# Optimization experiments

Hardware: AMD Instinct MI355X
Metric: run time of the kernel (lower is better)

## Reference

```python
import jax, jax.numpy as jnp
import numpy as np

HEADS = 8
KEY_DIM = 64
VALUE_DIM = 64


def setup_inputs() -> dict:
    key = jax.random.key(0)
    ks = jax.random.split(key, 6)
    B, I, O, T, S = 2, 512, 512, 2048, 2048
    E = KEY_DIM * HEADS  # 512
    Ev = VALUE_DIM * HEADS  # 512
    return {
        "x": jax.random.normal(ks[0], (B, I, T), dtype=jnp.float32),
        "y": jax.random.normal(ks[1], (B, O, S), dtype=jnp.float32),
        "mask": jnp.zeros((T, S), dtype=jnp.float32),
        "Wk": jax.random.normal(ks[2], (E, I), dtype=jnp.float32) * (I ** -0.5),
        "Wv": jax.random.normal(ks[3], (Ev, I), dtype=jnp.float32) * (I ** -0.5),
        "Wq": jax.random.normal(ks[4], (E, O), dtype=jnp.float32) * (O ** -0.5),
        "W": jax.random.normal(ks[5], (O, Ev), dtype=jnp.float32) * (Ev ** -0.5),
        "b": jnp.zeros((O,), dtype=jnp.float32),
    }


def reference(x, y, mask, Wk, Wv, Wq, W, b):
    B, I, T = x.shape
    S = y.shape[2]
    H, dk, dv = HEADS, KEY_DIM, VALUE_DIM
    scaling = dk ** -0.5
    # 1x1 Conv1d projections == channel GEMMs; reshape (B, H*d, L) -> (B*H, d, L)
    keys = jnp.einsum('ei,bit->bet', Wk, x).reshape(B * H, dk, T)
    values = jnp.einsum('ei,bit->bet', Wv, x).reshape(B * H, dv, T)
    queries = jnp.einsum('eo,bos->bes', Wq, y).reshape(B * H, dk, S)
    # scores: [B*H, T, S]
    dot = jnp.einsum('bkt,bks->bts', keys, queries)
    dot = dot + mask[None, :, :]
    # torch Softmax(1) on [bh, T, S] normalizes over T (keys axis);
    # note: scaling applied AFTER mask add, as in the original.
    attention = jax.nn.softmax(scaling * dot, axis=1)
    # weighted values: [B*H, dv, S] -> [B, H*dv, S]
    output = jnp.einsum('bvt,bts->bvs', values, attention).reshape(B, H * dv, S)
    # final Linear over channel dim applied to (B, S, H*dv)
    return jnp.einsum('bvs,ov->bso', output, W) + b
```

## Files before the change

kernel.cpp:

```cpp
#include <hip/hip_runtime.h>
#include <stdint.h>

typedef unsigned short u16;
typedef unsigned int u32;

#define B_    2
#define DK    64
#define T_    2048
#define S_    2048
#define CI    512
#define CO    512
#define E_    512

typedef short  short8 __attribute__((ext_vector_type(8)));
typedef __bf16 bf16x8 __attribute__((ext_vector_type(8)));
typedef float  f32x4  __attribute__((ext_vector_type(4)));

static __device__ __forceinline__ u16 f2bf(float f) {
    return __builtin_bit_cast(u16, (__bf16)f);
}

static __device__ __forceinline__ float bf2f(u16 h) {
    return __uint_as_float((u32)h << 16);
}

static __device__ __forceinline__ short8 ld8(const u16* p) {
    return *(const short8*)p;
}

static __device__ __forceinline__ f32x4 mfma_bf16(short8 a, short8 b, f32x4 c) {
    return __builtin_amdgcn_mfma_f32_16x16x32_bf16(
        __builtin_bit_cast(bf16x8, a), __builtin_bit_cast(bf16x8, b), c, 0, 0, 0);
}

__global__ __launch_bounds__(256) void k_prep(const float* __restrict__ x, const float* __restrict__ y,
                                              const float* __restrict__ wk, const float* __restrict__ wv,
                                              const float* __restrict__ wq, const float* __restrict__ wf,
                                              const float* __restrict__ mask,
                                              u16* __restrict__ xt, u16* __restrict__ yt,
                                              u16* __restrict__ wkb, u16* __restrict__ wvb,
                                              u16* __restrict__ wqb, u16* __restrict__ wfb,
                                              u16* __restrict__ mt, u32* __restrict__ mflag) {
    __shared__ float tile[32][33];
    int bid = blockIdx.x;
    if (bid < 4096) {
        int bx = bid & 63, by = (bid >> 6) & 15, bz = bid >> 10;
        int tsel = bz >> 1, b = bz & 1;
        const float* src = tsel ? y : x;
        u16* dst = tsel ? yt : xt;
        int t0 = bx * 32, i0 = by * 32;
        int tx = threadIdx.x & 31, ty = threadIdx.x >> 5;
#pragma unroll
        for (int r = 0; r < 4; r++)
            tile[ty + r * 8][tx] = src[(size_t)(b * CI + i0 + ty + r * 8) * T_ + t0 + tx];
        __syncthreads();
#pragma unroll
        for (int r = 0; r < 4; r++)
            dst[(size_t)(b * T_ + t0 + ty + r * 8) * CI + i0 + tx] = f2bf(tile[tx][ty + r * 8]);
    } else if (bid < 4608) {
        int off = ((bid - 4096) * 256 + threadIdx.x) * 8;
        int w = off >> 18, r = off & 262143;
        const float* s = (w == 0) ? wk : (w == 1) ? wv : (w == 2) ? wq : wf;
        u16* d = (w == 0) ? wkb : (w == 1) ? wvb : (w == 2) ? wqb : wfb;
        float4 a0 = *(const float4*)(s + r);
        float4 a1 = *(const float4*)(s + r + 4);
        short8 o;
        o[0] = f2bf(a0.x); o[1] = f2bf(a0.y); o[2] = f2bf(a0.z); o[3] = f2bf(a0.w);
        o[4] = f2bf(a1.x); o[5] = f2bf(a1.y); o[6] = f2bf(a1.z); o[7] = f2bf(a1.w);
        *(short8*)(d + r) = o;
    } else {
        int mb = bid - 4608;
        int t0 = (mb & 63) * 32, s0 = (mb >> 6) * 32;
        int tx = threadIdx.x & 31, ty = threadIdx.x >> 5;
        const float msc = 0.125f * 1.44269504088896f;
        bool nz = false;
#pragma unroll
        for (int r = 0; r < 4; r++) {
            float v = mask[(size_t)(t0 + ty + r * 8) * S_ + s0 + tx];
            tile[ty + r * 8][tx] = v;
            nz |= (v != 0.0f);
        }
        if (mflag && __any(nz) && (threadIdx.x & 63) == 0)
            atomicOr(mflag, 1u);
        __syncthreads();
#pragma unroll
        for (int r = 0; r < 4; r++)
            mt[(size_t)(s0 + ty + r * 8) * T_ + t0 + tx] = f2bf(tile[tx][ty + r * 8] * msc);
    }
}

__global__ __launch_bounds__(256) void k_proj3(const u16* __restrict__ xt, const u16* __restrict__ yt,
                                               const u16* __restrict__ wkb, const u16* __restrict__ wvb,
                                               const u16* __restrict__ wqb,
                                               u16* __restrict__ ktd, u16* __restrict__ vtd,
                                               u16* __restrict__ qtd, int p_base) {
    int bi = blockIdx.x;
    int p = p_base + (bi >> 8);
    int r = bi & 255;
    int et = r & 3, tt = r >> 2;
    int wv = threadIdx.x >> 6, lane = threadIdx.x & 63;
    int col = lane & 15, q = lane >> 4;
    int b = tt >> 5;
    int t0 = (tt & 31) * 64 + (wv >> 1) * 32;
    int e0 = et * 128 + (wv & 1) * 64;
    const u16* src = (p == 0) ? yt : xt;
    const u16* wb  = (p == 0) ? wqb : (p == 1) ? wkb : wvb;
    const u16* ap0 = src + (size_t)(b * T_ + t0 + col) * CI + q * 8;
    const u16* bp0 = wb + (size_t)(e0 + col) * CI + q * 8;
    f32x4 acc[2][4] = {};
    short8 a0 = ld8(ap0), a1 = ld8(ap0 + 16 * CI);
    short8 b0 = ld8(bp0), b1 = ld8(bp0 + 16 * CI);
    short8 b2 = ld8(bp0 + 32 * CI), b3 = ld8(bp0 + 48 * CI);
#pragma unroll
    for (int ks = 0; ks < 16; ks++) {
        short8 na0, na1, nb0, nb1, nb2, nb3;
        if (ks < 15) {
            na0 = ld8(ap0 + (ks + 1) * 32);
            na1 = ld8(ap0 + 16 * CI + (ks + 1) * 32);
            nb0 = ld8(bp0 + (ks + 1) * 32);
            nb1 = ld8(bp0 + 16 * CI + (ks + 1) * 32);
            nb2 = ld8(bp0 + 32 * CI + (ks + 1) * 32);
            nb3 = ld8(bp0 + 48 * CI + (ks + 1) * 32);
        }
        acc[0][0] = mfma_bf16(a0, b0, acc[0][0]); acc[1][0] = mfma_bf16(a1, b0, acc[1][0]);
        acc[0][1] = mfma_bf16(a0, b1, acc[0][1]); acc[1][1] = mfma_bf16(a1, b1, acc[1][1]);
        acc[0][2] = mfma_bf16(a0, b2, acc[0][2]); acc[1][2] = mfma_bf16(a1, b2, acc[1][2]);
        acc[0][3] = mfma_bf16(a0, b3, acc[0][3]); acc[1][3] = mfma_bf16(a1, b3, acc[1][3]);
        if (ks < 15) {
            a0 = na0; a1 = na1; b0 = nb0; b1 = nb1; b2 = nb2; b3 = nb3;
        }
    }
    float qs = (p == 0) ? 0.180336880f : 1.0f;
    u16* dst = (p == 0) ? qtd : (p == 1) ? ktd : vtd;
    if (p < 2) {
#pragma unroll
        for (int mt = 0; mt < 2; mt++)
#pragma unroll
            for (int nt = 0; nt < 4; nt++) {
                int e = e0 + nt * 16 + col, h = e >> 6, k = e & 63;
                u16* dp = dst + ((size_t)(b * 8 + h) * T_ + t0 + mt * 16 + q * 4) * DK + k;
                dp[0] = f2bf(acc[mt][nt][0] * qs);
                dp[DK] = f2bf(acc[mt][nt][1] * qs);
                dp[2 * DK] = f2bf(acc[mt][nt][2] * qs);
                dp[3 * DK] = f2bf(acc[mt][nt][3] * qs);
            }
    } else {
#pragma unroll
        for (int mt = 0; mt < 2; mt++)
#pragma unroll
            for (int nt = 0; nt < 4; nt++) {
                int e = e0 + nt * 16 + col, h = e >> 6, v = e & 63;
                uint2 pk;
                pk.x = f2bf(acc[mt][nt][0]) | ((u32)f2bf(acc[mt][nt][1]) << 16);
                pk.y = f2bf(acc[mt][nt][2]) | ((u32)f2bf(acc[mt][nt][3]) << 16);
                *(uint2*)(dst + ((size_t)(b * 8 + h) * DK + v) * T_ + t0 + mt * 16 + q * 4) = pk;
            }
    }
}


#define ATTN_ITER_M(T0, KC, MC4, MCF, KN, MN4, MNF, TN)  do {                       \
    short8 vb0 = ld8(vbase + (T0));                                                 \
    short8 vb1 = ld8(vbase + 16 * (size_t)T_ + (T0));                               \
    short8 vb2 = ld8(vbase + 32 * (size_t)T_ + (T0));                               \
    short8 vb3 = ld8(vbase + 48 * (size_t)T_ + (T0));                               \
    f32x4 s0g[4], s1g[4];                                                           \
    __builtin_amdgcn_s_setprio(1);                                                  \
    _Pragma("unroll") for (int g = 0; g < 4; g++) {                                 \
        f32x4 z = {};                                                               \
        s0g[g] = mfma_bf16(KC[0], qa[g][0], z);                                     \
        s0g[g] = mfma_bf16(KC[1], qa[g][1], s0g[g]);                                \
        s1g[g] = mfma_bf16(KC[2], qa[g][0], z);                                     \
        s1g[g] = mfma_bf16(KC[3], qa[g][1], s1g[g]);                                \
    }                                                                               \
    __builtin_amdgcn_s_setprio(0);                                                  \
    KN[0] = ld8(kbase + (size_t)(TN) * DK);                                         \
    KN[1] = ld8(kbase + (size_t)(TN) * DK + 32);                                    \
    KN[2] = ld8(kbase + (size_t)((TN) + 4) * DK);                                   \
    KN[3] = ld8(kbase + (size_t)((TN) + 4) * DK + 32);                              \
    if constexpr (MODE == 1) {                                                      \
        _Pragma("unroll") for (int g = 0; g < 4; g++) {                             \
            MN4[g][0] = *(const ushort4*)(mtb[g] + (TN));                           \
            MN4[g][1] = *(const ushort4*)(mtb[g] + (TN) + 4);                       \
        }                                                                           \
    } else {                                                                        \
        _Pragma("unroll") for (int g = 0; g < 4; g++)                               \
        _Pragma("unroll") for (int st = 0; st < 2; st++)                            \
        _Pragma("unroll") for (int rr = 0; rr < 4; rr++)                            \
            MNF[g][st * 4 + rr] =                                                   \
                mbs[g][(size_t)((TN) + q * 8 + st * 4 + rr) * S_] * msc;            \
    }                                                                               \
    _Pragma("unroll") for (int g = 0; g < 4; g++) {                                 \
        bf16x8 pbv;                                                                 \
        float lsum = 0.f;                                                           \
        _Pragma("unroll") for (int i = 0; i < 8; i++) {                             \
            float sv = (i < 4) ? s0g[g][i & 3] : s1g[g][i & 3];                     \
            float mv;                                                               \
            if constexpr (MODE == 1)                                                \
                mv = bf2f(((const u16*)&MC4[g][i >> 2])[i & 3]);                    \
            else                                                                    \
                mv = MCF[g][i];                                                     \
            float p = __builtin_amdgcn_exp2f(sv + mv);                              \
            lsum += p;                                                              \
            pbv[i] = (__bf16)p;                                                     \
        }                                                                           \
        l_part[g] += lsum;                                                          \
        short8 pa = __builtin_bit_cast(short8, pbv);                                \
        __builtin_amdgcn_s_setprio(1);                                              \
        oacc[g][0] = mfma_bf16(vb0, pa, oacc[g][0]);                                \
        oacc[g][1] = mfma_bf16(vb1, pa, oacc[g][1]);                                \
        oacc[g][2] = mfma_bf16(vb2, pa, oacc[g][2]);                                \
        oacc[g][3] = mfma_bf16(vb3, pa, oacc[g][3]);                                \
        __builtin_amdgcn_s_setprio(0);                                              \
    }                                                                               \
} while (0)

#define NM_PAIR(G0, KC, VC)  do {                                                   \
    f32x4 sa[2], sb[2];                                                             \
    __builtin_amdgcn_s_setprio(1);                                                  \
    _Pragma("unroll") for (int u = 0; u < 2; u++) {                                 \
        f32x4 z = {};                                                               \
        sa[u] = mfma_bf16(KC[0], qa[(G0) + u][0], z);                               \
        sa[u] = mfma_bf16(KC[1], qa[(G0) + u][1], sa[u]);                           \
        sb[u] = mfma_bf16(KC[2], qa[(G0) + u][0], z);                               \
        sb[u] = mfma_bf16(KC[3], qa[(G0) + u][1], sb[u]);                           \
    }                                                                               \
    __builtin_amdgcn_s_setprio(0);                                                  \
    _Pragma("unroll") for (int u = 0; u < 2; u++) {                                 \
        int g = (G0) + u;                                                           \
        bf16x8 pbv;                                                                 \
        float lsum = 0.f;                                                           \
        _Pragma("unroll") for (int i = 0; i < 8; i++) {                             \
            float sv = (i < 4) ? sa[u][i & 3] : sb[u][i & 3];                       \
            float p = __builtin_amdgcn_exp2f(sv);                                   \
            lsum += p;                                                              \
            pbv[i] = (__bf16)p;                                                     \
        }                                                                           \
        l_part[g] += lsum;                                                          \
        short8 pa = __builtin_bit_cast(short8, pbv);                                \
        __builtin_amdgcn_s_setprio(1);                                              \
        oacc[g][0] = mfma_bf16(VC[0], pa, oacc[g][0]);                              \
        oacc[g][1] = mfma_bf16(VC[1], pa, oacc[g][1]);                              \
        oacc[g][2] = mfma_bf16(VC[2], pa, oacc[g][2]);                              \
        oacc[g][3] = mfma_bf16(VC[3], pa, oacc[g][3]);                              \
        __builtin_amdgcn_s_setprio(0);                                              \
    }                                                                               \
} while (0)

#define ATTN_ITER_NM(KC, VC, KN, VN, TN)  do {                                      \
    NM_PAIR(0, KC, VC);                                                             \
    KN[0] = ld8(kbase + (size_t)(TN) * DK);                                         \
    KN[1] = ld8(kbase + (size_t)(TN) * DK + 32);                                    \
    KN[2] = ld8(kbase + (size_t)((TN) + 4) * DK);                                   \
    KN[3] = ld8(kbase + (size_t)((TN) + 4) * DK + 32);                              \
    VN[0] = ld8(vbase + (TN));                                                      \
    VN[1] = ld8(vbase + 16 * (size_t)T_ + (TN));                                    \
    VN[2] = ld8(vbase + 32 * (size_t)T_ + (TN));                                    \
    VN[3] = ld8(vbase + 48 * (size_t)T_ + (TN));                                    \
    NM_PAIR(2, KC, VC);                                                             \
} while (0)

template<int MODE>
__global__ __launch_bounds__(512, 2) void k_attn(const u16* __restrict__ kt, const u16* __restrict__ qt,
                                                 const u16* __restrict__ vt, const float* __restrict__ mask,
                                                 const u16* __restrict__ mt, const u32* __restrict__ mflag,
                                                 u16* __restrict__ oa) {
    __shared__ struct { float O[8][16][68]; float L[8][16]; } Sm;
    int wv = threadIdx.x >> 6, lane = threadIdx.x & 63;
    int col = lane & 15, q = lane >> 4;
    int bid = blockIdx.x;
    int j = bid >> 3;
    int bh = (bid & 7) * 2 + (j >> 5);
    int s_base = (j & 31) * 64;
    int sg = s_base + col;
    const int t_begin = wv * (T_ / 8);
    const int t_end = t_begin + (T_ / 8);
    short8 qa[4][2];
#pragma unroll
    for (int g = 0; g < 4; g++) {
        const u16* qp = qt + (size_t)(bh * S_ + sg + g * 16) * DK + q * 8;
        qa[g][0] = ld8(qp);
        qa[g][1] = ld8(qp + 32);
    }
    int tperm = ((col >> 2) << 3) | (col & 3);
    const u16* kbase = kt + (size_t)bh * T_ * DK + (size_t)tperm * DK + q * 8;
    const u16* vbase = vt + (size_t)bh * DK * T_ + (size_t)col * T_ + q * 8;
    float l_part[4] = {0.f, 0.f, 0.f, 0.f};
    f32x4 oacc[4][4] = {};
    const float msc = 0.180336880f;

    int use_mask = mflag ? (int)*mflag : 1;

    if (use_mask == 0) {
        short8 kA[4], kB[4], vA[4], vB[4];
        kA[0] = ld8(kbase + (size_t)t_begin * DK);
        kA[1] = ld8(kbase + (size_t)t_begin * DK + 32);
        kA[2] = ld8(kbase + (size_t)(t_begin + 4) * DK);
        kA[3] = ld8(kbase + (size_t)(t_begin + 4) * DK + 32);
        vA[0] = ld8(vbase + t_begin);
        vA[1] = ld8(vbase + 16 * (size_t)T_ + t_begin);
        vA[2] = ld8(vbase + 32 * (size_t)T_ + t_begin);
        vA[3] = ld8(vbase + 48 * (size_t)T_ + t_begin);
        for (int t0 = t_begin; t0 < t_end; t0 += 64) {
            ATTN_ITER_NM(kA, vA, kB, vB, t0 + 32);
            int tn2 = (t0 + 64 < t_end) ? (t0 + 64) : t_begin;
            ATTN_ITER_NM(kB, vB, kA, vA, tn2);
        }
    } else {
        const float* mbs[4];
        const u16* mtb[4];
#pragma unroll
        for (int g = 0; g < 4; g++) {
            mbs[g] = mask + sg + g * 16;
            mtb[g] = mt + (size_t)(sg + g * 16) * T_ + q * 8;
        }
        short8 kA[4], kB[4];
        ushort4 mA4[4][2], mB4[4][2];
        float mAf[4][8], mBf[4][8];
        kA[0] = ld8(kbase + (size_t)t_begin * DK);
        kA[1] = ld8(kbase + (size_t)t_begin * DK + 32);
        kA[2] = ld8(kbase + (size_t)(t_begin + 4) * DK);
        kA[3] = ld8(kbase + (size_t)(t_begin + 4) * DK + 32);
        if constexpr (MODE == 1) {
#pragma unroll
            for (int g = 0; g < 4; g++) {
                mA4[g][0] = *(const ushort4*)(mtb[g] + t_begin);
                mA4[g][1] = *(const ushort4*)(mtb[g] + t_begin + 4);
            }
        } else {
#pragma unroll
            for (int g = 0; g < 4; g++)
#pragma unroll
                for (int st = 0; st < 2; st++)
#pragma unroll
                    for (int rr = 0; rr < 4; rr++)
                        mAf[g][st * 4 + rr] =
                            mbs[g][(size_t)(t_begin + q * 8 + st * 4 + rr) * S_] * msc;
        }
        for (int t0 = t_begin; t0 < t_end; t0 += 64) {
            ATTN_ITER_M(t0, kA, mA4, mAf, kB, mB4, mBf, t0 + 32);
            int tn2 = (t0 + 64 < t_end) ? (t0 + 64) : t_begin;
            ATTN_ITER_M(t0 + 32, kB, mB4, mBf, kA, mA4, mAf, tn2);
        }
    }

#pragma unroll
    for (int g = 0; g < 4; g++) {
        float lr = l_part[g];
        lr += __shfl_xor(lr, 16);
        lr += __shfl_xor(lr, 32);
        l_part[g] = lr;
    }

    int b = bh >> 3, h = bh & 7;
    __syncthreads();
#pragma unroll
    for (int g = 0; g < 4; g++) {
#pragma unroll
        for (int nt = 0; nt < 4; nt++)
            *(f32x4*)&Sm.O[wv][col][nt * 16 + q * 4] = oacc[g][nt];
        if (lane < 16)
            Sm.L[wv][lane] = l_part[g];
        __syncthreads();
#pragma unroll
        for (int e = 0; e < 2; e++) {
            int f = (int)threadIdx.x + e * 512;
            int s = f >> 6, v = f & 63;
            float acc = 0.f, lt = 0.f;
#pragma unroll
            for (int c = 0; c < 8; c++) {
                acc += Sm.O[c][s][v];
                lt += Sm.L[c][s];
            }
            oa[(size_t)(b * S_ + s_base + g * 16 + s) * E_ + h * DK + v] = f2bf(acc / lt);
        }
        __syncthreads();
    }
}

__global__ __launch_bounds__(256) void k_final(const u16* __restrict__ oa, const u16* __restrict__ wfb,
                                               const float* __restrict__ bias, float* __restrict__ out) {
    int bi = blockIdx.x;
    int et = bi & 7, tt = bi >> 3;
    int wv = threadIdx.x >> 6, lane = threadIdx.x & 63;
    int col = lane & 15, q = lane >> 4;
    int b = tt >> 5;
    int s0 = (tt & 31) * 64 + (wv >> 1) * 32;
    int o0 = et * 64 + (wv & 1) * 32;
    const u16* ap0 = oa + (size_t)(b * S_ + s0 + col) * E_ + q * 8;
    const u16* bp0 = wfb + (size_t)(o0 + col) * E_ + q * 8;
    f32x4 acc[2][2] = {};
    short8 a0 = ld8(ap0), a1 = ld8(ap0 + 16 * E_);
    short8 b0 = ld8(bp0), b1 = ld8(bp0 + 16 * E_);
#pragma unroll
    for (int ks = 0; ks < 16; ks++) {
        short8 na0, na1, nb0, nb1;
        if (ks < 15) {
            na0 = ld8(ap0 + (ks + 1) * 32);
            na1 = ld8(ap0 + 16 * E_ + (ks + 1) * 32);
            nb0 = ld8(bp0 + (ks + 1) * 32);
            nb1 = ld8(bp0 + 16 * E_ + (ks + 1) * 32);
        }
        acc[0][0] = mfma_bf16(a0, b0, acc[0][0]); acc[1][0] = mfma_bf16(a1, b0, acc[1][0]);
        acc[0][1] = mfma_bf16(a0, b1, acc[0][1]); acc[1][1] = mfma_bf16(a1, b1, acc[1][1]);
        if (ks < 15) {
            a0 = na0; a1 = na1; b0 = nb0; b1 = nb1;
        }
    }
#pragma unroll
    for (int mt = 0; mt < 2; mt++)
#pragma unroll
        for (int nt = 0; nt < 2; nt++) {
            int o = o0 + nt * 16 + col;
            float bn = bias[o];
#pragma unroll
            for (int r = 0; r < 4; r++) {
                int s = s0 + mt * 16 + q * 4 + r;
                out[(size_t)(b * S_ + s) * CO + o] = acc[mt][nt][r] + bn;
            }
        }
}

extern "C" void kernel_launch(void* const* d_in, const int* in_sizes, int n_in,
                              void* d_out, int out_size, void* d_ws, size_t ws_size,
                              hipStream_t stream) {
    const float* x    = (const float*)d_in[0];
    const float* y    = (const float*)d_in[1];
    const float* mask = (const float*)d_in[2];
    const float* Wk   = (const float*)d_in[3];
    const float* Wv   = (const float*)d_in[4];
    const float* Wq   = (const float*)d_in[5];
    const float* Wf   = (const float*)d_in[6];
    const float* bias = (const float*)d_in[7];
    float* out = (float*)d_out;

    u16* ws = (u16*)d_ws;
    u16* XT  = ws;
    u16* YT  = XT + 2097152;
    u16* WKB = YT + 2097152;
    u16* WVB = WKB + 262144;
    u16* WQB = WVB + 262144;
    u16* WFB = WQB + 262144;
    u16* KT  = WFB + 262144;
    u16* QT  = KT + 2097152;
    u16* MT  = QT + 2097152;
    u16* VTs = MT + 4194304;
    u32* MF  = (u32*)(VTs + 2097152);
    u16* OA  = XT;

    int use_mt   = (ws_size >= (size_t)27262976) ? 1 : 0;
    int has_vt   = (ws_size >= (size_t)31457280) ? 1 : 0;
    int has_flag = (ws_size >= (size_t)31457344) ? 1 : 0;
    u16* VT = has_vt ? VTs : YT;
    u32* MFp = (use_mt && has_flag) ? MF : (u32*)nullptr;

    if (MFp)
        hipMemsetAsync(MFp, 0, 4, stream);
    k_prep<<<use_mt ? 8704 : 4608, 256, 0, stream>>>(x, y, Wk, Wv, Wq, Wf, mask,
                                                     XT, YT, WKB, WVB, WQB, WFB, MT, MFp);
    if (has_vt) {
        k_proj3<<<768, 256, 0, stream>>>(XT, YT, WKB, WVB, WQB, KT, VT, QT, 0);
    } else {
        k_proj3<<<512, 256, 0, stream>>>(XT, YT, WKB, WVB, WQB, KT, VT, QT, 0);
        k_proj3<<<256, 256, 0, stream>>>(XT, YT, WKB, WVB, WQB, KT, VT, QT, 2);
    }
    if (use_mt)
        k_attn<1><<<512, 512, 0, stream>>>(KT, QT, VT, mask, MT, MFp, OA);
    else
        k_attn<0><<<512, 512, 0, stream>>>(KT, QT, VT, mask, MT, MFp, OA);
    k_final<<<512, 256, 0, stream>>>(OA, WFB, bias, out);
}
```

Before: 202.4 us.

## Shrink projection and final GEMM tiles; restructure no-mask attention V loads

The projection kernel's per-wave tile drops from 32x64 to 32x32 and the final GEMM's from 32x32 to 16x32, doubling the grid sizes to give more blocks on the GPU. The no-mask attention path stops double-buffering V registers one iteration ahead. It now loads V at the start of each iteration, computes all four score groups before issuing the next K prefetch, and then runs the PV MFMAs. This cuts register pressure and raises parallelism, at the cost of more redundant global loads per FLOP and less latency hiding for V.

```diff
diff --git a/kernel.cpp b/kernel.cpp
--- a/kernel.cpp
+++ b/kernel.cpp
@@ -95,39 +95,34 @@
                                                u16* __restrict__ ktd, u16* __restrict__ vtd,
                                                u16* __restrict__ qtd, int p_base) {
     int bi = blockIdx.x;
-    int p = p_base + (bi >> 8);
-    int r = bi & 255;
-    int et = r & 3, tt = r >> 2;
+    int p = p_base + (bi >> 9);
+    int r = bi & 511;
+    int et = r & 7, tt = r >> 3;
     int wv = threadIdx.x >> 6, lane = threadIdx.x & 63;
     int col = lane & 15, q = lane >> 4;
     int b = tt >> 5;
     int t0 = (tt & 31) * 64 + (wv >> 1) * 32;
-    int e0 = et * 128 + (wv & 1) * 64;
+    int e0 = et * 64 + (wv & 1) * 32;
     const u16* src = (p == 0) ? yt : xt;
     const u16* wb  = (p == 0) ? wqb : (p == 1) ? wkb : wvb;
     const u16* ap0 = src + (size_t)(b * T_ + t0 + col) * CI + q * 8;
     const u16* bp0 = wb + (size_t)(e0 + col) * CI + q * 8;
-    f32x4 acc[2][4] = {};
+    f32x4 acc[2][2] = {};
     short8 a0 = ld8(ap0), a1 = ld8(ap0 + 16 * CI);
     short8 b0 = ld8(bp0), b1 = ld8(bp0 + 16 * CI);
-    short8 b2 = ld8(bp0 + 32 * CI), b3 = ld8(bp0 + 48 * CI);
 #pragma unroll
     for (int ks = 0; ks < 16; ks++) {
-        short8 na0, na1, nb0, nb1, nb2, nb3;
+        short8 na0, na1, nb0, nb1;
         if (ks < 15) {
             na0 = ld8(ap0 + (ks + 1) * 32);
             na1 = ld8(ap0 + 16 * CI + (ks + 1) * 32);
             nb0 = ld8(bp0 + (ks + 1) * 32);
             nb1 = ld8(bp0 + 16 * CI + (ks + 1) * 32);
-            nb2 = ld8(bp0 + 32 * CI + (ks + 1) * 32);
-            nb3 = ld8(bp0 + 48 * CI + (ks + 1) * 32);
         }
         acc[0][0] = mfma_bf16(a0, b0, acc[0][0]); acc[1][0] = mfma_bf16(a1, b0, acc[1][0]);
         acc[0][1] = mfma_bf16(a0, b1, acc[0][1]); acc[1][1] = mfma_bf16(a1, b1, acc[1][1]);
-        acc[0][2] = mfma_bf16(a0, b2, acc[0][2]); acc[1][2] = mfma_bf16(a1, b2, acc[1][2]);
-        acc[0][3] = mfma_bf16(a0, b3, acc[0][3]); acc[1][3] = mfma_bf16(a1, b3, acc[1][3]);
         if (ks < 15) {
-            a0 = na0; a1 = na1; b0 = nb0; b1 = nb1; b2 = nb2; b3 = nb3;
+            a0 = na0; a1 = na1; b0 = nb0; b1 = nb1;
         }
     }
     float qs = (p == 0) ? 0.180336880f : 1.0f;
@@ -136,7 +131,7 @@
 #pragma unroll
         for (int mt = 0; mt < 2; mt++)
 #pragma unroll
-            for (int nt = 0; nt < 4; nt++) {
+            for (int nt = 0; nt < 2; nt++) {
                 int e = e0 + nt * 16 + col, h = e >> 6, k = e & 63;
                 u16* dp = dst + ((size_t)(b * 8 + h) * T_ + t0 + mt * 16 + q * 4) * DK + k;
                 dp[0] = f2bf(acc[mt][nt][0] * qs);
@@ -148,7 +143,7 @@
 #pragma unroll
         for (int mt = 0; mt < 2; mt++)
 #pragma unroll
-            for (int nt = 0; nt < 4; nt++) {
+            for (int nt = 0; nt < 2; nt++) {
                 int e = e0 + nt * 16 + col, h = e >> 6, v = e & 63;
                 uint2 pk;
                 pk.x = f2bf(acc[mt][nt][0]) | ((u32)f2bf(acc[mt][nt][1]) << 16);
@@ -215,23 +210,30 @@
     }                                                                               \
 } while (0)
 
-#define NM_PAIR(G0, KC, VC)  do {                                                   \
-    f32x4 sa[2], sb[2];                                                             \
+#define ATTN_ITER_NM(T0, KC, KN, TN)  do {                                          \
+    short8 vb0 = ld8(vbase + (T0));                                                 \
+    short8 vb1 = ld8(vbase + 16 * (size_t)T_ + (T0));                               \
+    short8 vb2 = ld8(vbase + 32 * (size_t)T_ + (T0));                               \
+    short8 vb3 = ld8(vbase + 48 * (size_t)T_ + (T0));                               \
+    f32x4 s0g[4], s1g[4];                                                           \
     __builtin_amdgcn_s_setprio(1);                                                  \
-    _Pragma("unroll") for (int u = 0; u < 2; u++) {                                 \
+    _Pragma("unroll") for (int g = 0; g < 4; g++) {                                 \
         f32x4 z = {};                                                               \
-        sa[u] = mfma_bf16(KC[0], qa[(G0) + u][0], z);                               \
-        sa[u] = mfma_bf16(KC[1], qa[(G0) + u][1], sa[u]);                           \
-        sb[u] = mfma_bf16(KC[2], qa[(G0) + u][0], z);                               \
-        sb[u] = mfma_bf16(KC[3], qa[(G0) + u][1], sb[u]);                           \
+        s0g[g] = mfma_bf16(KC[0], qa[g][0], z);                                     \
+        s0g[g] = mfma_bf16(KC[1], qa[g][1], s0g[g]);                                \
+        s1g[g] = mfma_bf16(KC[2], qa[g][0], z);                                     \
+        s1g[g] = mfma_bf16(KC[3], qa[g][1], s1g[g]);                                \
     }                                                                               \
     __builtin_amdgcn_s_setprio(0);                                                  \
-    _Pragma("unroll") for (int u = 0; u < 2; u++) {                                 \
-        int g = (G0) + u;                                                           \
+    KN[0] = ld8(kbase + (size_t)(TN) * DK);                                         \
+    KN[1] = ld8(kbase + (size_t)(TN) * DK + 32);                                    \
+    KN[2] = ld8(kbase + (size_t)((TN) + 4) * DK);                                   \
+    KN[3] = ld8(kbase + (size_t)((TN) + 4) * DK + 32);                              \
+    _Pragma("unroll") for (int g = 0; g < 4; g++) {                                 \
         bf16x8 pbv;                                                                 \
         float lsum = 0.f;                                                           \
         _Pragma("unroll") for (int i = 0; i < 8; i++) {                             \
-            float sv = (i < 4) ? sa[u][i & 3] : sb[u][i & 3];                       \
+            float sv = (i < 4) ? s0g[g][i & 3] : s1g[g][i & 3];                     \
             float p = __builtin_amdgcn_exp2f(sv);                                   \
             lsum += p;                                                              \
             pbv[i] = (__bf16)p;                                                     \
@@ -239,25 +241,12 @@
         l_part[g] += lsum;                                                          \
         short8 pa = __builtin_bit_cast(short8, pbv);                                \
         __builtin_amdgcn_s_setprio(1);                                              \
-        oacc[g][0] = mfma_bf16(VC[0], pa, oacc[g][0]);                              \
-        oacc[g][1] = mfma_bf16(VC[1], pa, oacc[g][1]);                              \
-        oacc[g][2] = mfma_bf16(VC[2], pa, oacc[g][2]);                              \
-        oacc[g][3] = mfma_bf16(VC[3], pa, oacc[g][3]);                              \
+        oacc[g][0] = mfma_bf16(vb0, pa, oacc[g][0]);                                \
+        oacc[g][1] = mfma_bf16(vb1, pa, oacc[g][1]);                                \
+        oacc[g][2] = mfma_bf16(vb2, pa, oacc[g][2]);                                \
+        oacc[g][3] = mfma_bf16(vb3, pa, oacc[g][3]);                                \
         __builtin_amdgcn_s_setprio(0);                                              \
     }                                                                               \
-} while (0)
-
-#define ATTN_ITER_NM(KC, VC, KN, VN, TN)  do {                                      \
-    NM_PAIR(0, KC, VC);                                                             \
-    KN[0] = ld8(kbase + (size_t)(TN) * DK);                                         \
-    KN[1] = ld8(kbase + (size_t)(TN) * DK + 32);                                    \
-    KN[2] = ld8(kbase + (size_t)((TN) + 4) * DK);                                   \
-    KN[3] = ld8(kbase + (size_t)((TN) + 4) * DK + 32);                              \
-    VN[0] = ld8(vbase + (TN));                                                      \
-    VN[1] = ld8(vbase + 16 * (size_t)T_ + (TN));                                    \
-    VN[2] = ld8(vbase + 32 * (size_t)T_ + (TN));                                    \
-    VN[3] = ld8(vbase + 48 * (size_t)T_ + (TN));                                    \
-    NM_PAIR(2, KC, VC);                                                             \
 } while (0)
 
 template<int MODE>
@@ -292,19 +281,15 @@
     int use_mask = mflag ? (int)*mflag : 1;
 
     if (use_mask == 0) {
-        short8 kA[4], kB[4], vA[4], vB[4];
+        short8 kA[4], kB[4];
         kA[0] = ld8(kbase + (size_t)t_begin * DK);
         kA[1] = ld8(kbase + (size_t)t_begin * DK + 32);
         kA[2] = ld8(kbase + (size_t)(t_begin + 4) * DK);
         kA[3] = ld8(kbase + (size_t)(t_begin + 4) * DK + 32);
-        vA[0] = ld8(vbase + t_begin);
-        vA[1] = ld8(vbase + 16 * (size_t)T_ + t_begin);
-        vA[2] = ld8(vbase + 32 * (size_t)T_ + t_begin);
-        vA[3] = ld8(vbase + 48 * (size_t)T_ + t_begin);
         for (int t0 = t_begin; t0 < t_end; t0 += 64) {
-            ATTN_ITER_NM(kA, vA, kB, vB, t0 + 32);
+            ATTN_ITER_NM(t0, kA, kB, t0 + 32);
             int tn2 = (t0 + 64 < t_end) ? (t0 + 64) : t_begin;
-            ATTN_ITER_NM(kB, vB, kA, vA, tn2);
+            ATTN_ITER_NM(t0 + 32, kB, kA, tn2);
         }
     } else {
         const float* mbs[4];
@@ -384,41 +369,38 @@
     int et = bi & 7, tt = bi >> 3;
     int wv = threadIdx.x >> 6, lane = threadIdx.x & 63;
     int col = lane & 15, q = lane >> 4;
-    int b = tt >> 5;
-    int s0 = (tt & 31) * 64 + (wv >> 1) * 32;
+    int b = tt >> 6;
+    int s0 = (tt & 63) * 32 + (wv >> 1) * 16;
     int o0 = et * 64 + (wv & 1) * 32;
     const u16* ap0 = oa + (size_t)(b * S_ + s0 + col) * E_ + q * 8;
     const u16* bp0 = wfb + (size_t)(o0 + col) * E_ + q * 8;
-    f32x4 acc[2][2] = {};
-    short8 a0 = ld8(ap0), a1 = ld8(ap0 + 16 * E_);
+    f32x4 acc[2] = {};
+    short8 a0 = ld8(ap0);
     short8 b0 = ld8(bp0), b1 = ld8(bp0 + 16 * E_);
 #pragma unroll
     for (int ks = 0; ks < 16; ks++) {
-        short8 na0, na1, nb0, nb1;
+        short8 na0, nb0, nb1;
         if (ks < 15) {
             na0 = ld8(ap0 + (ks + 1) * 32);
-            na1 = ld8(ap0 + 16 * E_ + (ks + 1) * 32);
             nb0 = ld8(bp0 + (ks + 1) * 32);
             nb1 = ld8(bp0 + 16 * E_ + (ks + 1) * 32);
         }
-        acc[0][0] = mfma_bf16(a0, b0, acc[0][0]); acc[1][0] = mfma_bf16(a1, b0, acc[1][0]);
-        acc[0][1] = mfma_bf16(a0, b1, acc[0][1]); acc[1][1] = mfma_bf16(a1, b1, acc[1][1]);
+        acc[0] = mfma_bf16(a0, b0, acc[0]);
+        acc[1] = mfma_bf16(a0, b1, acc[1]);
         if (ks < 15) {
-            a0 = na0; a1 = na1; b0 = nb0; b1 = nb1;
-        }
-    }
-#pragma unroll
-    for (int mt = 0; mt < 2; mt++)
-#pragma unroll
-        for (int nt = 0; nt < 2; nt++) {
-            int o = o0 + nt * 16 + col;
-            float bn = bias[o];
-#pragma unroll
-            for (int r = 0; r < 4; r++) {
-                int s = s0 + mt * 16 + q * 4 + r;
-                out[(size_t)(b * S_ + s) * CO + o] = acc[mt][nt][r] + bn;
-            }
-        }
+            a0 = na0; b0 = nb0; b1 = nb1;
+        }
+    }
+#pragma unroll
+    for (int nt = 0; nt < 2; nt++) {
+        int o = o0 + nt * 16 + col;
+        float bn = bias[o];
+#pragma unroll
+        for (int r = 0; r < 4; r++) {
+            int s = s0 + q * 4 + r;
+            out[(size_t)(b * S_ + s) * CO + o] = acc[nt][r] + bn;
+        }
+    }
 }
 
 extern "C" void kernel_launch(void* const* d_in, const int* in_sizes, int n_in,
@@ -459,14 +441,14 @@
     k_prep<<<use_mt ? 8704 : 4608, 256, 0, stream>>>(x, y, Wk, Wv, Wq, Wf, mask,
                                                      XT, YT, WKB, WVB, WQB, WFB, MT, MFp);
     if (has_vt) {
-        k_proj3<<<768, 256, 0, stream>>>(XT, YT, WKB, WVB, WQB, KT, VT, QT, 0);
+        k_proj3<<<1536, 256, 0, stream>>>(XT, YT, WKB, WVB, WQB, KT, VT, QT, 0);
     } else {
-        k_proj3<<<512, 256, 0, stream>>>(XT, YT, WKB, WVB, WQB, KT, VT, QT, 0);
-        k_proj3<<<256, 256, 0, stream>>>(XT, YT, WKB, WVB, WQB, KT, VT, QT, 2);
+        k_proj3<<<1024, 256, 0, stream>>>(XT, YT, WKB, WVB, WQB, KT, VT, QT, 0);
+        k_proj3<<<512, 256, 0, stream>>>(XT, YT, WKB, WVB, WQB, KT, VT, QT, 2);
     }
     if (use_mt)
         k_attn<1><<<512, 512, 0, stream>>>(KT, QT, VT, mask, MT, MFp, OA);
     else
         k_attn<0><<<512, 512, 0, stream>>>(KT, QT, VT, mask, MT, MFp, OA);
-    k_final<<<512, 256, 0, stream>>>(OA, WFB, bias, out);
-}
+    k_final<<<1024, 256, 0, stream>>>(OA, WFB, bias, out);
+}
```

Result: slower. 212.1 us (+4.8%).
